# Kernel optimization log

Hardware: AMD Instinct MI355X
Metric: run time of the kernel (lower is better)

The kernel has to match this reference:

```python
import jax, jax.numpy as jnp
import numpy as np
from jax.scipy.special import logsumexp

B, S, K = 512, 2048, 17

def setup_inputs() -> dict:
    key = jax.random.key(0)
    k_em, k_lab, k_len, k_st, k_en, k_tr = jax.random.split(key, 6)
    emissions = jax.random.normal(k_em, (B, S, K), dtype=jnp.float32)
    labels = jax.random.randint(k_lab, (B, S), 0, K, dtype=jnp.int64).astype(jnp.int32)
    # ragged valid-prefix mask; torchcrf requires mask[:, 0] to be all True
    lengths = jax.random.randint(k_len, (B,), 1, S + 1)
    attention_mask = (jnp.arange(S)[None, :] < lengths[:, None]).astype(jnp.int32)
    # CRF params (torchcrf inits uniform(-0.1, 0.1))
    start_transitions = jax.random.uniform(k_st, (K,), minval=-0.1, maxval=0.1, dtype=jnp.float32)
    end_transitions = jax.random.uniform(k_en, (K,), minval=-0.1, maxval=0.1, dtype=jnp.float32)
    transitions = jax.random.uniform(k_tr, (K, K), minval=-0.1, maxval=0.1, dtype=jnp.float32)
    return {
        "emissions": emissions,
        "start_transitions": start_transitions,
        "end_transitions": end_transitions,
        "transitions": transitions,
        "labels": labels,
        "attention_mask": attention_mask,
    }


def _crf_neg_log_likelihood(emissions, start_transitions, end_transitions, transitions,
                            labels, mask_bool):
    # emissions: [B,S,K], labels: [B,S] int, mask_bool: [B,S] bool (mask[:,0] all True)
    mask_f = mask_bool.astype(emissions.dtype)
    b_idx = jnp.arange(emissions.shape[0])

    # ---- numerator: score of the gold path ----
    first_tags = labels[:, 0]                                  # [B]
    num = start_transitions[first_tags] + emissions[b_idx, 0, first_tags]
    prev_tags = labels[:, :-1]                                 # [B,S-1]
    cur_tags = labels[:, 1:]                                   # [B,S-1]
    emit_t = jnp.take_along_axis(emissions[:, 1:, :], cur_tags[..., None], axis=-1)[..., 0]
    step_scores = transitions[prev_tags, cur_tags] + emit_t    # [B,S-1]
    num = num + jnp.sum(step_scores * mask_f[:, 1:], axis=1)
    seq_ends = jnp.sum(mask_bool, axis=1).astype(jnp.int32) - 1  # [B]
    last_tags = jnp.take_along_axis(labels, seq_ends[:, None], axis=1)[:, 0]
    num = num + end_transitions[last_tags]

    # ---- denominator: log partition via forward algorithm (lax.scan over time) ----
    alpha0 = start_transitions[None, :] + emissions[:, 0, :]   # [B,K]

    def step(alpha, xs):
        emit, m = xs                                           # emit [B,K], m [B] bool
        # alpha[b, i] + transitions[i, j] + emit[b, j] -> logsumexp over i
        nxt = logsumexp(alpha[:, :, None] + transitions[None, :, :] + emit[:, None, :], axis=1)
        alpha = jnp.where(m[:, None], nxt, alpha)
        return alpha, None

    em_seq = jnp.swapaxes(emissions[:, 1:, :], 0, 1)           # [S-1,B,K]
    m_seq = jnp.swapaxes(mask_bool[:, 1:], 0, 1)               # [S-1,B]
    alpha, _ = jax.lax.scan(step, alpha0, (em_seq, m_seq))
    log_z = logsumexp(alpha + end_transitions[None, :], axis=1)  # [B]

    llh = num - log_z
    return -jnp.mean(llh)  # torchcrf reduction='mean', loss = -crf(...)


def reference(emissions, start_transitions, end_transitions, transitions, labels, attention_mask):
    mask_bool = attention_mask.astype(bool) & (labels >= 0)
    labels_c = jnp.where(labels == -100, 0, labels)
    loss = _crf_neg_log_likelihood(emissions, start_transitions, end_transitions,
                                   transitions, labels_c, mask_bool)
    return loss, emissions
```

## Files before the change

### kernel.cpp

```cpp
#include <hip/hip_runtime.h>
#include <cstddef>

#define NB 512
#define NS 2048
#define NK 17
#define CL 8
#define NW 4
#define HT 1024
#define SP 8
#define NLT (HT + SP)
#define CHUNKD 37
#define ROWD 9
#define LDS_DW ((NLT / 4) * CHUNKD)

typedef __fp16 h2 __attribute__((ext_vector_type(2)));
typedef float  f4 __attribute__((ext_vector_type(4)));
union UH { unsigned int u; h2 h; };

__global__ void prep_k(const float* __restrict__ trans, const int* __restrict__ attn,
                       unsigned int* __restrict__ Mg, int* __restrict__ lens) {
    __shared__ int red[4];
    const int tid = threadIdx.x;
    if (blockIdx.x == 0) {
        if (tid < 9 * NK) {
            int kk = tid / NK, n = tid % NK;
            float lo = __expf(trans[(2 * kk) * NK + n]);
            float hi = (kk < 8) ? __expf(trans[(2 * kk + 1) * NK + n]) : 0.f;
            UH u; u.h = __builtin_amdgcn_cvt_pkrtz(lo, hi);
            Mg[tid] = u.u;
        }
        return;
    }
    const int b = blockIdx.x - 1;
    const int4* __restrict__ a4 = (const int4*)(attn + (size_t)b * NS);
    int4 x = a4[tid];
    int4 y = a4[tid + 256];
    int s = x.x + x.y + x.z + x.w + y.x + y.y + y.z + y.w;
#pragma unroll
    for (int off = 32; off >= 1; off >>= 1) s += __shfl_down(s, off, 64);
    if ((tid & 63) == 0) red[tid >> 6] = s;
    __syncthreads();
    if (tid == 0) lens[b] = red[0] + red[1] + red[2] + red[3];
}

__global__ __launch_bounds__(256, 4) void crf_fused(
    const float* __restrict__ emis,
    const float* __restrict__ startT,
    const float* __restrict__ endT,
    const float* __restrict__ trans,
    const int*   __restrict__ labels,
    const int*   __restrict__ lens,
    const unsigned int* __restrict__ Mg,
    float*       __restrict__ outE,
    float*       __restrict__ out)
{
    __shared__ unsigned int expE[LDS_DW];
    float* red = (float*)expE;

    const int tid = threadIdx.x;
    const int b  = blockIdx.x >> 1;
    const int h  = blockIdx.x & 1;
    const int T0 = h << 10;
    const int len = lens[b];

    const size_t ebOff = (size_t)b * NS * NK;
    const float* __restrict__ eb = emis + ebOff;
    float*       __restrict__ ob = outE + ebOff;
    const int*   __restrict__ lb = labels + (size_t)b * NS;

    const int endF = (T0 + HT) * NK;
    const int ownF = T0 * NK;

    if (T0 >= len) {
        int g = ownF + tid * 4;
        f4 v = {0.f, 0.f, 0.f, 0.f};
        if (g < endF) v = *(const f4*)(eb + g);
        while (g < endF) {
            int gn = g + 1024;
            f4 vn = v;
            if (gn < endF) vn = *(const f4*)(eb + gn);
            __builtin_nontemporal_store(v, (f4*)(ob + g));
            v = vn; g = gn;
        }
        return;
    }

    const int loadT0 = (h == 0) ? 0 : (T0 - SP);
    const int baseF  = loadT0 * NK;
    const int lenF   = len * NK;

    {
        int g = baseF + tid * 4;
        int t4  = (int)((unsigned)g / 17u);
        int n4  = g - t4 * 17;
        int lt4 = t4 - (T0 - SP);
        f4 v = {0.f, 0.f, 0.f, 0.f};
        if (g < endF) v = *(const f4*)(eb + g);
        while (g < endF) {
            const int gn = g + 1024;
            f4 vn = v;
            if (gn < endF) vn = *(const f4*)(eb + gn);
            if (g >= ownF) __builtin_nontemporal_store(v, (f4*)(ob + g));
            if (g < lenF) {
                float ev[4] = {v.x, v.y, v.z, v.w};
                int lt = lt4, nn = n4;
#pragma unroll
                for (int u = 0; u < 4; ++u) {
                    int ha = ((lt >> 2) * CHUNKD + (lt & 3) * ROWD) * 2 + nn;
                    ((__fp16*)expE)[ha] = (__fp16)__expf(ev[u]);
                    ++nn; if (nn == 17) { nn = 0; ++lt; }
                }
            }
            lt4 += 60; n4 += 4; if (n4 >= 17) { n4 -= 17; ++lt4; }
            v = vn; g = gn;
        }
    }
    __syncthreads();

    float numA = 0.f, zc = 0.f;

    if (tid >= 128) {
        int t = T0 + (tid - 128);
#pragma unroll
        for (int j = 0; j < 8; ++j, t += 128) {
            if (t < len) {
                int la = lb[t];
                numA += eb[(size_t)t * NK + la];
                numA += (t == 0) ? startT[la] : trans[lb[t - 1] * NK + la];
                if (t == len - 1) numA += endT[la];
            }
        }
    } else if (T0 + ((tid & 64) << 3) < len) {
        const int gc = h * 128 + tid;
        const int t0 = gc * CL;
        const int cE = (len - 1) >> 3;
        float logscale = 0.f, endlog = 0.f;
        bool hasEnd = false;
        h2 wh[9];
        {
            const __fp16 iv = (__fp16)(1.f / NK);
#pragma unroll
            for (int kk = 0; kk < 9; ++kk) { wh[kk].x = iv; wh[kk].y = iv; }
            wh[8].y = (__fp16)0.f;
        }

        if (gc == 0) {
            float wf[NK]; float ssum = 0.f;
            const int bdw = (SP >> 2) * CHUNKD;
#pragma unroll
            for (int k = 0; k < 9; ++k) {
                UH u; u.u = expE[bdw + k];
                int n = 2 * k;
                wf[n] = __expf(startT[n]) * (float)u.h.x;
                if (n + 1 < NK) wf[n + 1] = __expf(startT[n + 1]) * (float)u.h.y;
            }
#pragma unroll
            for (int n = 0; n < NK; ++n) ssum += wf[n];
            float r = 1.f / ssum;
            logscale = __logf(ssum);
#pragma unroll
            for (int kk = 0; kk < 8; ++kk)
                wh[kk] = __builtin_amdgcn_cvt_pkrtz(wf[2 * kk] * r, wf[2 * kk + 1] * r);
            wh[8] = __builtin_amdgcn_cvt_pkrtz(wf[16] * r, 0.f);
            if (len == 1) {
                float sd = 0.f;
#pragma unroll
                for (int n = 0; n < NK; ++n) sd += wf[n] * __expf(endT[n]);
                endlog = __logf(sd);
                hasEnd = true;
            }
        }

#pragma unroll 1
        for (int i = 0; i < CL + NW; ++i) {
            int t = t0 - NW + i;
            bool active = (t >= 1);
            int ta = active ? t : 1;
            int lt = ta - (T0 - SP);
            int bdw = (lt >> 2) * CHUNKD + (lt & 3) * ROWD;
            float ex[NK + 1];
#pragma unroll
            for (int k = 0; k < 9; ++k) {
                UH u; u.u = expE[bdw + k];
                ex[2 * k]     = (float)u.h.x;
                ex[2 * k + 1] = (float)u.h.y;
            }
            if (gc != 0 && t == t0) logscale = 0.f;

            float acc[NK];
#pragma unroll
            for (int n = 0; n < NK; ++n) acc[n] = 0.f;
#pragma unroll
            for (int kk = 0; kk < 9; ++kk) {
                h2 w = wh[kk];
#pragma unroll
                for (int n = 0; n < NK; ++n) {
                    UH u; u.u = Mg[kk * NK + n];
                    acc[n] = __builtin_amdgcn_fdot2(w, u.h, acc[n], false);
                }
            }
            float wf[NK]; float ssum = 0.f;
#pragma unroll
            for (int n = 0; n < NK; ++n) {
                float w = acc[n] * ex[n];
                wf[n] = w;
                ssum += w;
            }
            float r  = __builtin_amdgcn_rcpf(ssum);
            float lg = __logf(ssum);
            if (active) {
                if (t >= t0 && t == len - 1) {
                    float sd = 0.f;
#pragma unroll
                    for (int n = 0; n < NK; ++n) sd += wf[n] * __expf(endT[n]);
                    endlog = logscale + __logf(sd);
                    hasEnd = true;
                }
                logscale += lg;
#pragma unroll
                for (int kk = 0; kk < 8; ++kk)
                    wh[kk] = __builtin_amdgcn_cvt_pkrtz(wf[2 * kk] * r, wf[2 * kk + 1] * r);
                wh[8] = __builtin_amdgcn_cvt_pkrtz(wf[16] * r, 0.f);
            }
        }

        zc = ((gc < cE) ? logscale : 0.f) + (hasEnd ? endlog : 0.f);
    }

    __syncthreads();
    red[tid] = numA - zc;
    __syncthreads();
    for (int k = 128; k >= 1; k >>= 1) { if (tid < k) red[tid] += red[tid + k]; __syncthreads(); }
    if (tid == 0) atomicAdd(out, -red[0] * (1.f / (float)NB));
}

extern "C" void kernel_launch(void* const* d_in, const int* in_sizes, int n_in,
                              void* d_out, int out_size, void* d_ws, size_t ws_size,
                              hipStream_t stream) {
    (void)in_sizes; (void)n_in; (void)out_size; (void)ws_size;
    const float* emis   = (const float*)d_in[0];
    const float* startT = (const float*)d_in[1];
    const float* endT   = (const float*)d_in[2];
    const float* trans  = (const float*)d_in[3];
    const int*   labels = (const int*)d_in[4];
    const int*   attn   = (const int*)d_in[5];
    float* out = (float*)d_out;
    unsigned int* Mg = (unsigned int*)d_ws;
    int* lens        = (int*)((char*)d_ws + 1024);

    (void)hipMemsetAsync(d_out, 0, sizeof(float), stream);
    prep_k<<<NB + 1, 256, 0, stream>>>(trans, attn, Mg, lens);
    crf_fused<<<NB * 2, 256, 0, stream>>>(emis, startT, endT, trans, labels,
                                          lens, Mg, out + 1, out);
}
```

Baseline: 166.7 us.

## Balance work by splitting valid chunks evenly across the two blocks per sequence

The two blocks per sequence used to split at a fixed timestep 1024, which left one block idle or overloaded whenever lengths were ragged. Each block now takes half of the valid 8-step chunks, with chunk and LDS offsets computed from the sequence length. The emissions pass-through copy is separated into a fixed, unrolled, software-pipelined copy of each block's half, and the exp/LDS fill covers only the valid chunk range. This cuts the critical-path recurrence per block, but it adds branching, and the copy now runs separately from the exp load, so some emission data is read twice.

```diff
diff --git a/kernel.cpp b/kernel.cpp
--- a/kernel.cpp
+++ b/kernel.cpp
@@ -60,56 +60,74 @@
     const int tid = threadIdx.x;
     const int b  = blockIdx.x >> 1;
     const int h  = blockIdx.x & 1;
-    const int T0 = h << 10;
     const int len = lens[b];
+
+    const int CT = (len + 7) >> 3;
+    const int C0 = (CT + 1) >> 1;
+    const int chunkBase = h ? C0 : 0;
+    const int chunkEnd  = h ? CT : C0;
+    const int ltBase = chunkBase * 8 - SP;
 
     const size_t ebOff = (size_t)b * NS * NK;
     const float* __restrict__ eb = emis + ebOff;
     float*       __restrict__ ob = outE + ebOff;
     const int*   __restrict__ lb = labels + (size_t)b * NS;
 
-    const int endF = (T0 + HT) * NK;
-    const int ownF = T0 * NK;
-
-    if (T0 >= len) {
-        int g = ownF + tid * 4;
-        f4 v = {0.f, 0.f, 0.f, 0.f};
-        if (g < endF) v = *(const f4*)(eb + g);
-        while (g < endF) {
-            int gn = g + 1024;
-            f4 vn = v;
-            if (gn < endF) vn = *(const f4*)(eb + gn);
-            __builtin_nontemporal_store(v, (f4*)(ob + g));
-            v = vn; g = gn;
-        }
-        return;
-    }
-
-    const int loadT0 = (h == 0) ? 0 : (T0 - SP);
-    const int baseF  = loadT0 * NK;
-    const int lenF   = len * NK;
-
     {
-        int g = baseF + tid * 4;
+        const int ownF = (h << 10) * NK;
+        const float* __restrict__ src = eb + ownF;
+        float*       __restrict__ dst = ob + ownF;
+        const int base = tid * 4;
+        f4 r0 = *(const f4*)(src + base);
+        f4 r1 = *(const f4*)(src + base + 1024);
+        f4 r2 = *(const f4*)(src + base + 2048);
+        f4 r3 = *(const f4*)(src + base + 3072);
+#pragma unroll
+        for (int k = 0; k < 3; ++k) {
+            const int o = k * 4096 + base;
+            f4 n0 = *(const f4*)(src + o + 4096);
+            f4 n1 = *(const f4*)(src + o + 5120);
+            f4 n2 = *(const f4*)(src + o + 6144);
+            f4 n3 = *(const f4*)(src + o + 7168);
+            __builtin_nontemporal_store(r0, (f4*)(dst + o));
+            __builtin_nontemporal_store(r1, (f4*)(dst + o + 1024));
+            __builtin_nontemporal_store(r2, (f4*)(dst + o + 2048));
+            __builtin_nontemporal_store(r3, (f4*)(dst + o + 3072));
+            r0 = n0; r1 = n1; r2 = n2; r3 = n3;
+        }
+        const int o = 12288 + base;
+        f4 n0 = *(const f4*)(src + o + 4096);
+        __builtin_nontemporal_store(r0, (f4*)(dst + o));
+        __builtin_nontemporal_store(r1, (f4*)(dst + o + 1024));
+        __builtin_nontemporal_store(r2, (f4*)(dst + o + 2048));
+        __builtin_nontemporal_store(r3, (f4*)(dst + o + 3072));
+        __builtin_nontemporal_store(n0, (f4*)(dst + o + 4096));
+    }
+
+    {
+        const int TL0   = h ? (C0 * 8 - SP) : 0;
+        const int Tstop = h ? len : (C0 * 8 < len ? C0 * 8 : len);
+        const int startF = TL0 * NK;
+        const int stopF  = Tstop * NK;
+        int g = startF + tid * 4;
         int t4  = (int)((unsigned)g / 17u);
         int n4  = g - t4 * 17;
-        int lt4 = t4 - (T0 - SP);
+        int lt4 = t4 - ltBase;
         f4 v = {0.f, 0.f, 0.f, 0.f};
-        if (g < endF) v = *(const f4*)(eb + g);
-        while (g < endF) {
+        if (g < stopF) v = *(const f4*)(eb + g);
+        while (g < stopF) {
             const int gn = g + 1024;
             f4 vn = v;
-            if (gn < endF) vn = *(const f4*)(eb + gn);
-            if (g >= ownF) __builtin_nontemporal_store(v, (f4*)(ob + g));
-            if (g < lenF) {
-                float ev[4] = {v.x, v.y, v.z, v.w};
-                int lt = lt4, nn = n4;
-#pragma unroll
-                for (int u = 0; u < 4; ++u) {
+            if (gn < stopF) vn = *(const f4*)(eb + gn);
+            float ev[4] = {v.x, v.y, v.z, v.w};
+            int lt = lt4, nn = n4;
+#pragma unroll
+            for (int u = 0; u < 4; ++u) {
+                if (g + u < stopF) {
                     int ha = ((lt >> 2) * CHUNKD + (lt & 3) * ROWD) * 2 + nn;
                     ((__fp16*)expE)[ha] = (__fp16)__expf(ev[u]);
-                    ++nn; if (nn == 17) { nn = 0; ++lt; }
                 }
+                ++nn; if (nn == 17) { nn = 0; ++lt; }
             }
             lt4 += 60; n4 += 4; if (n4 >= 17) { n4 -= 17; ++lt4; }
             v = vn; g = gn;
@@ -120,18 +138,21 @@
     float numA = 0.f, zc = 0.f;
 
     if (tid >= 128) {
-        int t = T0 + (tid - 128);
+        const int tg0 = chunkBase * 8;
+        const int tg1 = h ? len : (C0 * 8 < len ? C0 * 8 : len);
+        int t = tg0 + (tid - 128);
 #pragma unroll
         for (int j = 0; j < 8; ++j, t += 128) {
-            if (t < len) {
+            if (t < tg1) {
                 int la = lb[t];
                 numA += eb[(size_t)t * NK + la];
                 numA += (t == 0) ? startT[la] : trans[lb[t - 1] * NK + la];
                 if (t == len - 1) numA += endT[la];
             }
         }
-    } else if (T0 + ((tid & 64) << 3) < len) {
-        const int gc = h * 128 + tid;
+    } else if (chunkBase + (tid & 64) < chunkEnd) {
+        const int gc = chunkBase + tid;
+        const bool owned = gc < chunkEnd;
         const int t0 = gc * CL;
         const int cE = (len - 1) >> 3;
         float logscale = 0.f, endlog = 0.f;
@@ -176,7 +197,7 @@
             int t = t0 - NW + i;
             bool active = (t >= 1);
             int ta = active ? t : 1;
-            int lt = ta - (T0 - SP);
+            int lt = ta - ltBase;
             int bdw = (lt >> 2) * CHUNKD + (lt & 3) * ROWD;
             float ex[NK + 1];
 #pragma unroll
@@ -209,7 +230,7 @@
             float r  = __builtin_amdgcn_rcpf(ssum);
             float lg = __logf(ssum);
             if (active) {
-                if (t >= t0 && t == len - 1) {
+                if (owned && t >= t0 && t == len - 1) {
                     float sd = 0.f;
 #pragma unroll
                     for (int n = 0; n < NK; ++n) sd += wf[n] * __expf(endT[n]);
@@ -224,7 +245,7 @@
             }
         }
 
-        zc = ((gc < cE) ? logscale : 0.f) + (hasEnd ? endlog : 0.f);
+        zc = owned ? (((gc < cE) ? logscale : 0.f) + (hasEnd ? endlog : 0.f)) : 0.f;
     }
 
     __syncthreads();
```

New measurement: 176.7 us. +6.0%, slower.
